# Optimization experiments

Measured on AMD Instinct MI355X. Metric: run time of the kernel, lower is better.

The kernel has to match this reference:

```python
import jax, jax.numpy as jnp
import numpy as np

EPS = 1e-8
TAU = 0.2
IOU_THR = 0.5
NEG = -1e9
N, C, H, D_FG, D_CLS = 8192, 1024, 256, 64, 128


def setup_inputs() -> dict:
    key = jax.random.key(0)
    ks = jax.random.split(key, 11)
    def lin(k, fan_in, fan_out):
        return jax.random.normal(k, (fan_in, fan_out), jnp.float32) / np.sqrt(fan_in)
    return {
        "roi_feats": jax.random.normal(ks[0], (N, C), jnp.float32),
        "labels": jax.random.randint(ks[1], (N,), 0, 21, jnp.int32).astype(jnp.int64),
        "ious": jax.random.uniform(ks[2], (N,), jnp.float32),
        "fg_w1": lin(ks[3], C, H), "fg_b1": jnp.zeros((H,), jnp.float32),
        "fg_w2": lin(ks[4], H, D_FG), "fg_b2": jnp.zeros((D_FG,), jnp.float32),
        "cls_w1": lin(ks[5], C, H), "cls_b1": jnp.zeros((H,), jnp.float32),
        "cls_w2": lin(ks[6], H, D_CLS), "cls_b2": jnp.zeros((D_CLS,), jnp.float32),
    }


def _project_normalize(x, w1, b1, w2, b2):
    h = jax.nn.relu(x @ w1 + b1)
    z = h @ w2 + b2
    norm = jnp.maximum(jnp.linalg.norm(z, axis=1, keepdims=True), EPS)
    return z / norm


def _forward(roi_feats, labels, ious, fg_w1, fg_b1, fg_w2, fg_b2, cls_w1, cls_b1, cls_w2, cls_b2):
    n = roi_feats.shape[0]
    z_fg = _project_normalize(roi_feats, fg_w1, fg_b1, fg_w2, fg_b2)
    z_cls = _project_normalize(roi_feats, cls_w1, cls_b1, cls_w2, cls_b2)

    ignore = labels == -1
    fg = (labels > 0) & ~ignore
    iou_weight = jnp.where(ious > IOU_THR, ious, 0.0)
    eye = jnp.eye(n, dtype=bool)

    # ---- fg/bg contrastive (bg_as_negatives_only=True) ----
    sim_fg = (z_fg @ z_fg.T) / TAU                       # [N,N]
    exp_sim = jnp.exp(sim_fg)
    denom = jnp.sum(exp_sim * (~eye).astype(jnp.float32), axis=1)
    pos = (fg & ~ignore)[None, :] & ~eye                 # positives: fg columns, no self
    n_pos = jnp.sum(pos, axis=1)
    numer = jnp.sum(exp_sim * pos.astype(jnp.float32), axis=1)
    # original computes den = denom + EPS then -log((numer+EPS)/(den+EPS))
    loss_i = -jnp.log((numer + EPS) / (denom + 2.0 * EPS))
    valid = (fg & ~ignore) & (n_pos > 0)
    w = iou_weight * valid.astype(jnp.float32)
    loss_fg_bg = jnp.sum(w * loss_i) / (jnp.sum(w) + EPS)

    # ---- class supervised contrastive ----
    sim_cls = (z_cls @ z_cls.T) / TAU
    sim_masked = jnp.where(eye, NEG, sim_cls)
    log_denom = jax.nn.logsumexp(sim_masked, axis=1)     # [N]
    log_p = jnp.where(eye, NEG, sim_cls - log_denom[:, None])
    # pos_mask keeps diagonal (as in original): same label, col not ignore, col label != 0
    posc = (labels[None, :] == labels[:, None]) & (~ignore)[None, :] & (labels[None, :] != 0)
    n_posc = jnp.sum(posc, axis=1).astype(jnp.float32)
    sum_log_p = jnp.sum(log_p * posc.astype(jnp.float32), axis=1)
    valid_c = (fg & ~ignore) & (n_posc > 0) & jnp.isfinite(log_denom)
    Lzi = jnp.where(valid_c, -sum_log_p / (n_posc + EPS), 0.0)
    wc = iou_weight * valid_c.astype(jnp.float32)
    loss_supcon = jnp.sum(wc * Lzi) / (jnp.sum(wc) + EPS)

    return jnp.stack([loss_fg_bg, loss_supcon])


def reference(roi_feats, labels, ious, fg_w1, fg_b1, fg_w2, fg_b2, cls_w1, cls_b1, cls_w2, cls_b2):
    return _forward(roi_feats, labels, ious, fg_w1, fg_b1, fg_w2, fg_b2, cls_w1, cls_b1, cls_w2, cls_b2)
```

## Files before the change

kernel.cpp:

```cpp
#include <hip/hip_runtime.h>


typedef __attribute__((ext_vector_type(8))) short bs8;
typedef __attribute__((ext_vector_type(4))) float f4;

#define MFMA_BF16(a, b, c) __builtin_amdgcn_mfma_f32_16x16x32_bf16((a), (b), (c), 0, 0, 0)

#if defined(__has_builtin)
#if __has_builtin(__builtin_amdgcn_exp2f)
#define EXP2F(x) __builtin_amdgcn_exp2f(x)
#endif
#endif
#ifndef EXP2F
#define EXP2F(x) exp2f(x)
#endif

#define K_LOG2E 7.2134752044448170f

__device__ __forceinline__ unsigned short f2bf(float f) {
  unsigned int u = __float_as_uint(f);
  u = (u + 0x7fffu + ((u >> 16) & 1u)) >> 16;
  return (unsigned short)u;
}
__device__ __forceinline__ float bf2f(unsigned short s) {
  return __uint_as_float(((unsigned int)s) << 16);
}

constexpr size_t O_W1T  = 0;
constexpr size_t O_W2TF = 1048576;
constexpr size_t O_W2TC = 1081344;
constexpr size_t O_H    = 1146880;
constexpr size_t O_ZF   = 9535488;
constexpr size_t O_ZC   = 10584064;
constexpr size_t O_SCLS = 12681216;
constexpr size_t O_ROWD = 12697600;
constexpr size_t O_ROWN = 12730368;
constexpr size_t O_ROWS = 12763136;
constexpr size_t O_SCAL = 12795904;
constexpr size_t O_HIST = 12795920;
constexpr size_t O_NFG  = 12796048;
constexpr int ZERO_WORDS = (int)((O_NFG + 4 - O_SCLS) / 4);

__global__ void __launch_bounds__(256) zero_kernel(float* __restrict__ p, int n) {
  int i = blockIdx.x * 256 + threadIdx.x;
  if (i < n) p[i] = 0.f;
}

__global__ void __launch_bounds__(256) transp_kernel(
    const float* __restrict__ fgw1, const float* __restrict__ clsw1,
    const float* __restrict__ fgw2, const float* __restrict__ clsw2,
    unsigned short* __restrict__ W1T, unsigned short* __restrict__ W2Tf,
    unsigned short* __restrict__ W2Tc) {
  __shared__ float tile[64][65];
  const int m = blockIdx.y;
  const float* src;
  unsigned short* dst;
  int R, C;
  if (m == 0)      { src = fgw1;  dst = W1T;              R = 1024; C = 256; }
  else if (m == 1) { src = clsw1; dst = W1T + 256 * 1024; R = 1024; C = 256; }
  else if (m == 2) { src = fgw2;  dst = W2Tf;             R = 256;  C = 64;  }
  else             { src = clsw2; dst = W2Tc;             R = 256;  C = 128; }
  const int cT = C >> 6;
  if (blockIdx.x >= (R >> 6) * cT) return;
  const int r0 = (blockIdx.x / cT) << 6, c0 = (blockIdx.x % cT) << 6;
  const int t = threadIdx.x;
  {
    const int rr = t >> 4, cc = (t & 15) << 2;
#pragma unroll
    for (int i = 0; i < 4; i++) {
      float4 v = *(const float4*)(src + (size_t)(r0 + rr + i * 16) * C + c0 + cc);
      tile[rr + i * 16][cc] = v.x; tile[rr + i * 16][cc + 1] = v.y;
      tile[rr + i * 16][cc + 2] = v.z; tile[rr + i * 16][cc + 3] = v.w;
    }
  }
  __syncthreads();
  {
    const int dr = t >> 2, dc = (t & 3) << 4;
    bs8 o0, o1;
#pragma unroll
    for (int j = 0; j < 8; j++) o0[j] = (short)f2bf(tile[dc + j][dr]);
#pragma unroll
    for (int j = 0; j < 8; j++) o1[j] = (short)f2bf(tile[dc + 8 + j][dr]);
    unsigned short* dp = dst + (size_t)(c0 + dr) * R + r0 + dc;
    *(bs8*)dp = o0;
    *(bs8*)(dp + 8) = o1;
  }
}

__global__ void __launch_bounds__(256) meta_kernel(const int* __restrict__ labels,
                                                   int* __restrict__ hist,
                                                   int* __restrict__ nfg) {
  __shared__ int sh[33];
  const int t = threadIdx.x;
  if (t < 33) sh[t] = 0;
  __syncthreads();
  int lab = labels[blockIdx.x * 256 + t];
  if (lab >= 0 && lab < 32) atomicAdd(&sh[lab], 1);
  if (lab > 0) atomicAdd(&sh[32], 1);
  __syncthreads();
  if (t < 32 && sh[t] > 0) atomicAdd(&hist[t], sh[t]);
  if (t == 32 && sh[32] > 0) atomicAdd(nfg, sh[32]);
}

__global__ void __launch_bounds__(256) gemm1_kernel(
    const float* __restrict__ X, const unsigned short* __restrict__ W1T,
    const float* __restrict__ b1f, const float* __restrict__ b1c,
    unsigned short* __restrict__ H) {
  __shared__ __align__(16) unsigned short lA[128 * 40];
  __shared__ __align__(16) unsigned short lB[64 * 40];
  const int t = threadIdx.x;
  const int w = t >> 6, lane = t & 63, ln = lane & 15, quad = lane >> 4;
  const int m0 = blockIdx.x * 128, n0 = blockIdx.y * 64;

  f4 acc[2][4];
#pragma unroll
  for (int rs = 0; rs < 2; rs++)
#pragma unroll
    for (int s = 0; s < 4; s++) acc[rs][s] = (f4){0.f, 0.f, 0.f, 0.f};

  for (int k0 = 0; k0 < 1024; k0 += 32) {
    __syncthreads();
#pragma unroll
    for (int i = 0; i < 2; i++) {
      int ch = t + i * 256;
      int r = ch >> 2, c = (ch & 3) * 8;
      const float* xp = X + (size_t)(m0 + r) * 1024 + k0 + c;
      float4 x0 = *(const float4*)xp;
      float4 x1 = *(const float4*)(xp + 4);
      bs8 av;
      av[0] = (short)f2bf(x0.x); av[1] = (short)f2bf(x0.y);
      av[2] = (short)f2bf(x0.z); av[3] = (short)f2bf(x0.w);
      av[4] = (short)f2bf(x1.x); av[5] = (short)f2bf(x1.y);
      av[6] = (short)f2bf(x1.z); av[7] = (short)f2bf(x1.w);
      *(bs8*)&lA[r * 40 + c] = av;
    }
    {
      int r = t >> 2, c = (t & 3) * 8;
      *(bs8*)&lB[r * 40 + c] = *(const bs8*)(W1T + (size_t)(n0 + r) * 1024 + k0 + c);
    }
    __syncthreads();
    bs8 af0 = *(const bs8*)&lA[(w * 32 + ln) * 40 + quad * 8];
    bs8 af1 = *(const bs8*)&lA[(w * 32 + 16 + ln) * 40 + quad * 8];
#pragma unroll
    for (int s = 0; s < 4; s++) {
      bs8 bf = *(const bs8*)&lB[(s * 16 + ln) * 40 + quad * 8];
      acc[0][s] = MFMA_BF16(af0, bf, acc[0][s]);
      acc[1][s] = MFMA_BF16(af1, bf, acc[1][s]);
    }
  }
#pragma unroll
  for (int s = 0; s < 4; s++) {
    int n = n0 + s * 16 + ln;
    float b = (n < 256) ? b1f[n] : b1c[n - 256];
#pragma unroll
    for (int rs = 0; rs < 2; rs++)
#pragma unroll
      for (int r = 0; r < 4; r++) {
        float v = fmaxf(acc[rs][s][r] + b, 0.f);
        H[(size_t)(m0 + w * 32 + rs * 16 + quad * 4 + r) * 512 + n] = f2bf(v);
      }
  }
}

__global__ void __launch_bounds__(256) gemm2_kernel(
    const unsigned short* __restrict__ H,
    const unsigned short* __restrict__ W2Tf, const unsigned short* __restrict__ W2Tc,
    const float* __restrict__ b2f, const float* __restrict__ b2c,
    unsigned short* __restrict__ Zf, unsigned short* __restrict__ Zc) {
  const int t = threadIdx.x;
  const int w = t >> 6, lane = t & 63, ln = lane & 15, quad = lane >> 4;
  const int rw = blockIdx.x * 32 + (w & 1) * 16;

  if (w < 2) {
    const unsigned short* hrow = H + (size_t)(rw + ln) * 512;
    f4 acc[4];
#pragma unroll
    for (int s = 0; s < 4; s++) acc[s] = (f4){0.f, 0.f, 0.f, 0.f};
#pragma unroll
    for (int ks = 0; ks < 8; ks++) {
      bs8 af = *(const bs8*)(hrow + ks * 32 + quad * 8);
#pragma unroll
      for (int s = 0; s < 4; s++) {
        bs8 bf = *(const bs8*)(W2Tf + (size_t)(s * 16 + ln) * 256 + ks * 32 + quad * 8);
        acc[s] = MFMA_BF16(af, bf, acc[s]);
      }
    }
    float ss[4] = {0.f, 0.f, 0.f, 0.f};
#pragma unroll
    for (int s = 0; s < 4; s++) {
      float b = b2f[s * 16 + ln];
#pragma unroll
      for (int r = 0; r < 4; r++) {
        acc[s][r] += b;
        ss[r] = fmaf(acc[s][r], acc[s][r], ss[r]);
      }
    }
#pragma unroll
    for (int r = 0; r < 4; r++) {
#pragma unroll
      for (int off = 1; off < 16; off <<= 1) ss[r] += __shfl_xor(ss[r], off, 64);
      float sc = 1.f / fmaxf(sqrtf(ss[r]), 1e-8f);
#pragma unroll
      for (int s = 0; s < 4; s++)
        Zf[(size_t)(rw + quad * 4 + r) * 64 + s * 16 + ln] = f2bf(acc[s][r] * sc);
    }
  } else {
    const unsigned short* hrow = H + (size_t)(rw + ln) * 512 + 256;
    f4 acc[8];
#pragma unroll
    for (int s = 0; s < 8; s++) acc[s] = (f4){0.f, 0.f, 0.f, 0.f};
#pragma unroll
    for (int ks = 0; ks < 8; ks++) {
      bs8 af = *(const bs8*)(hrow + ks * 32 + quad * 8);
#pragma unroll
      for (int s = 0; s < 8; s++) {
        bs8 bf = *(const bs8*)(W2Tc + (size_t)(s * 16 + ln) * 256 + ks * 32 + quad * 8);
        acc[s] = MFMA_BF16(af, bf, acc[s]);
      }
    }
    float ss[4] = {0.f, 0.f, 0.f, 0.f};
#pragma unroll
    for (int s = 0; s < 8; s++) {
      float b = b2c[s * 16 + ln];
#pragma unroll
      for (int r = 0; r < 4; r++) {
        acc[s][r] += b;
        ss[r] = fmaf(acc[s][r], acc[s][r], ss[r]);
      }
    }
#pragma unroll
    for (int r = 0; r < 4; r++) {
#pragma unroll
      for (int off = 1; off < 16; off <<= 1) ss[r] += __shfl_xor(ss[r], off, 64);
      float sc = 1.f / fmaxf(sqrtf(ss[r]), 1e-8f);
#pragma unroll
      for (int s = 0; s < 8; s++)
        Zc[(size_t)(rw + quad * 4 + r) * 128 + s * 16 + ln] = f2bf(acc[s][r] * sc);
    }
  }
}

__global__ void __launch_bounds__(128) scls_kernel(const unsigned short* __restrict__ Zc,
                                                   const int* __restrict__ labels,
                                                   float* __restrict__ Scls) {
  const int c = blockIdx.x + 1;
  const int t = threadIdx.x;
  const int r0 = blockIdx.y * 256;
  float acc = 0.f;
#pragma unroll 4
  for (int r = r0; r < r0 + 256; r++) {
    if (labels[r] == c) acc += bf2f(Zc[(size_t)r * 128 + t]);
  }
  atomicAdd(&Scls[c * 128 + t], acc);
}

__global__ void __launch_bounds__(256) sim_kernel(
    const unsigned short* __restrict__ Zf, const unsigned short* __restrict__ Zc,
    const int* __restrict__ labels,
    float* __restrict__ rowD, float* __restrict__ rowN, float* __restrict__ rowS) {
  const int bi = blockIdx.x, d = blockIdx.y;
  if (d == 32 && bi >= 32) return;
  const int bj = (bi + d) & 63;
  const bool diag = (d == 0);

  __shared__ __align__(16) unsigned short sZf[64 * 72];
  __shared__ __align__(16) unsigned short sZc[64 * 136];
  __shared__ float sFg[64];
  __shared__ float sCol[4][2][4][16][3];
  const int t = threadIdx.x;
  const int w = t >> 6, lane = t & 63, ln = lane & 15, quad = lane >> 4;
  const int rbase = bi * 128 + w * 32;

  bs8 afg[2][2], acl[2][4];
  float fgr[2][4];
#pragma unroll
  for (int rs = 0; rs < 2; rs++) {
    const unsigned short* zf = Zf + (size_t)(rbase + rs * 16 + ln) * 64;
    const unsigned short* zc = Zc + (size_t)(rbase + rs * 16 + ln) * 128;
#pragma unroll
    for (int s = 0; s < 2; s++) afg[rs][s] = *(const bs8*)(zf + s * 32 + quad * 8);
#pragma unroll
    for (int s = 0; s < 4; s++) acl[rs][s] = *(const bs8*)(zc + s * 32 + quad * 8);
#pragma unroll
    for (int r = 0; r < 4; r++)
      fgr[rs][r] = (labels[rbase + rs * 16 + quad * 4 + r] > 0) ? 1.f : 0.f;
  }

  float dacc[2][4] = {}, nacc[2][4] = {}, sacc[2][4] = {};
  float cdacc[2][4] = {}, cnacc[2][4] = {}, csacc[2][4] = {};

#pragma unroll
  for (int ct = 0; ct < 2; ct++) {
    const int c0 = bj * 128 + ct * 64;
    __syncthreads();
#pragma unroll
    for (int i = 0; i < 2; i++) {
      int ch = t + i * 256;
      int j = ch >> 3, c8 = (ch & 7) * 8;
      *(bs8*)&sZf[j * 72 + c8] = *(const bs8*)(Zf + (size_t)(c0 + j) * 64 + c8);
    }
#pragma unroll
    for (int i = 0; i < 4; i++) {
      int ch = t + i * 256;
      int j = ch >> 4, c8 = (ch & 15) * 8;
      *(bs8*)&sZc[j * 136 + c8] = *(const bs8*)(Zc + (size_t)(c0 + j) * 128 + c8);
    }
    if (t < 64) sFg[t] = (labels[c0 + t] > 0) ? 1.f : 0.f;
    __syncthreads();

#pragma unroll
    for (int s = 0; s < 4; s++) {
      const int lcol = s * 16 + ln;
      const float fgc = sFg[lcol];
      bs8 b0 = *(const bs8*)&sZf[lcol * 72 + quad * 8];
      bs8 b1 = *(const bs8*)&sZf[lcol * 72 + 32 + quad * 8];
#pragma unroll
      for (int rs = 0; rs < 2; rs++) {
        f4 c = {0.f, 0.f, 0.f, 0.f};
        c = MFMA_BF16(afg[rs][0], b0, c);
        c = MFMA_BF16(afg[rs][1], b1, c);
#pragma unroll
        for (int r = 0; r < 4; r++) {
          float e = EXP2F(c[r] * K_LOG2E);
          dacc[rs][r] += e;
          nacc[rs][r] = fmaf(fgc, e, nacc[rs][r]);
          cdacc[ct][s] += e;
          cnacc[ct][s] = fmaf(fgr[rs][r], e, cnacc[ct][s]);
        }
      }
      bs8 bc0 = *(const bs8*)&sZc[lcol * 136 + quad * 8];
      bs8 bc1 = *(const bs8*)&sZc[lcol * 136 + 32 + quad * 8];
      bs8 bc2 = *(const bs8*)&sZc[lcol * 136 + 64 + quad * 8];
      bs8 bc3 = *(const bs8*)&sZc[lcol * 136 + 96 + quad * 8];
#pragma unroll
      for (int rs = 0; rs < 2; rs++) {
        f4 c = {0.f, 0.f, 0.f, 0.f};
        c = MFMA_BF16(acl[rs][0], bc0, c);
        c = MFMA_BF16(acl[rs][1], bc1, c);
        c = MFMA_BF16(acl[rs][2], bc2, c);
        c = MFMA_BF16(acl[rs][3], bc3, c);
#pragma unroll
        for (int r = 0; r < 4; r++) {
          float e = EXP2F(c[r] * K_LOG2E);
          sacc[rs][r] += e;
          csacc[ct][s] += e;
        }
      }
    }
  }

#pragma unroll
  for (int rs = 0; rs < 2; rs++)
#pragma unroll
    for (int r = 0; r < 4; r++) {
      float dv = dacc[rs][r], nv = nacc[rs][r], sv = sacc[rs][r];
#pragma unroll
      for (int off = 1; off < 16; off <<= 1) {
        dv += __shfl_xor(dv, off, 64);
        nv += __shfl_xor(nv, off, 64);
        sv += __shfl_xor(sv, off, 64);
      }
      if (ln == 0) {
        int row = rbase + rs * 16 + quad * 4 + r;
        atomicAdd(&rowD[row], dv);
        atomicAdd(&rowN[row], nv);
        atomicAdd(&rowS[row], sv);
      }
    }

  if (!diag) {
#pragma unroll
    for (int ct = 0; ct < 2; ct++)
#pragma unroll
      for (int s = 0; s < 4; s++) {
        float dv = cdacc[ct][s], nv = cnacc[ct][s], sv = csacc[ct][s];
#pragma unroll
        for (int off = 16; off < 64; off <<= 1) {
          dv += __shfl_xor(dv, off, 64);
          nv += __shfl_xor(nv, off, 64);
          sv += __shfl_xor(sv, off, 64);
        }
        if (quad == 0) {
          sCol[w][ct][s][ln][0] = dv;
          sCol[w][ct][s][ln][1] = nv;
          sCol[w][ct][s][ln][2] = sv;
        }
      }
    __syncthreads();
    if (t < 128) {
      const int ct = t >> 6, s = (t >> 4) & 3, lm = t & 15;
      float dv = 0.f, nv = 0.f, sv = 0.f;
#pragma unroll
      for (int ww = 0; ww < 4; ww++) {
        dv += sCol[ww][ct][s][lm][0];
        nv += sCol[ww][ct][s][lm][1];
        sv += sCol[ww][ct][s][lm][2];
      }
      const int col = bj * 128 + t;
      atomicAdd(&rowD[col], dv);
      atomicAdd(&rowN[col], nv);
      atomicAdd(&rowS[col], sv);
    }
  }
}

__global__ void __launch_bounds__(256) finalize_kernel(
    const unsigned short* __restrict__ Zf, const unsigned short* __restrict__ Zc,
    const int* __restrict__ labels, const float* __restrict__ ious,
    const float* __restrict__ rowD, const float* __restrict__ rowN,
    const float* __restrict__ rowS, const float* __restrict__ Scls,
    const int* __restrict__ hist, const int* __restrict__ nfg,
    float* __restrict__ scal) {
  __shared__ float red[4][4];
  const int t = threadIdx.x, w = t >> 6, lane = t & 63;
  float aw0 = 0.f, al0 = 0.f, aw1 = 0.f, al1 = 0.f;
  const int NFG = *nfg;
  for (int it = 0; it < 16; it++) {
    const int i = it * 512 + blockIdx.x * 4 + w;
    const int lab = labels[i];
    if (lab > 0 && lab < 32) {
      const float iou = ious[i];
      const float iw = (iou > 0.5f) ? iou : 0.f;
      float dot = 0.f, ssq = 0.f;
#pragma unroll
      for (int p = 0; p < 2; p++) {
        const int k = lane + p * 64;
        const float z = bf2f(Zc[(size_t)i * 128 + k]);
        dot = fmaf(z, Scls[lab * 128 + k], dot);
        ssq = fmaf(z, z, ssq);
      }
      float zf = bf2f(Zf[(size_t)i * 64 + lane]);
      float ssqf = zf * zf;
#pragma unroll
      for (int off = 1; off < 64; off <<= 1) {
        dot += __shfl_xor(dot, off, 64);
        ssq += __shfl_xor(ssq, off, 64);
        ssqf += __shfl_xor(ssqf, off, 64);
      }
      if (lane == 0) {
        const float ef = EXP2F(K_LOG2E * ssqf);
        if (NFG - 1 > 0) {
          const float D = rowD[i] - ef;
          const float Nn = rowN[i] - ef;
          const float loss = logf(D + 2e-8f) - logf(Nn + 1e-8f);
          aw0 += iw;
          al0 += iw * loss;
        }
        const int npc = hist[lab];
        if (npc > 0) {
          const float S = rowS[i] - EXP2F(K_LOG2E * ssq);
          const float logden = logf(S);
          const float slp = (dot - ssq) * 5.0f - (float)(npc - 1) * logden - 1e9f;
          aw1 += iw;
          al1 += iw * (-slp / ((float)npc + 1e-8f));
        }
      }
    }
  }
  if (lane == 0) { red[w][0] = aw0; red[w][1] = al0; red[w][2] = aw1; red[w][3] = al1; }
  __syncthreads();
  if (t < 4) atomicAdd(&scal[t], red[0][t] + red[1][t] + red[2][t] + red[3][t]);
}

__global__ void writeout_kernel(const float* __restrict__ scal, float* __restrict__ out) {
  if (threadIdx.x == 0) {
    out[0] = scal[1] / (scal[0] + 1e-8f);
    out[1] = scal[3] / (scal[2] + 1e-8f);
  }
}

extern "C" void kernel_launch(void* const* d_in, const int* in_sizes, int n_in,
                              void* d_out, int out_size, void* d_ws, size_t ws_size,
                              hipStream_t stream) {
  (void)in_sizes; (void)n_in; (void)out_size; (void)ws_size;
  const float* roi    = (const float*)d_in[0];
  const int*   labels = (const int*)d_in[1];
  const float* ious   = (const float*)d_in[2];
  const float* fgw1   = (const float*)d_in[3];
  const float* fgb1   = (const float*)d_in[4];
  const float* fgw2   = (const float*)d_in[5];
  const float* fgb2   = (const float*)d_in[6];
  const float* clsw1  = (const float*)d_in[7];
  const float* clsb1  = (const float*)d_in[8];
  const float* clsw2  = (const float*)d_in[9];
  const float* clsb2  = (const float*)d_in[10];

  char* ws = (char*)d_ws;
  unsigned short* W1T  = (unsigned short*)(ws + O_W1T);
  unsigned short* W2Tf = (unsigned short*)(ws + O_W2TF);
  unsigned short* W2Tc = (unsigned short*)(ws + O_W2TC);
  unsigned short* Hb   = (unsigned short*)(ws + O_H);
  unsigned short* Zf   = (unsigned short*)(ws + O_ZF);
  unsigned short* Zc   = (unsigned short*)(ws + O_ZC);
  float* Scls = (float*)(ws + O_SCLS);
  float* rowD = (float*)(ws + O_ROWD);
  float* rowN = (float*)(ws + O_ROWN);
  float* rowS = (float*)(ws + O_ROWS);
  float* scal = (float*)(ws + O_SCAL);
  int* hist = (int*)(ws + O_HIST);
  int* nfg  = (int*)(ws + O_NFG);
  float* out = (float*)d_out;

  hipLaunchKernelGGL(zero_kernel, dim3((ZERO_WORDS + 255) / 256), dim3(256), 0, stream,
                     (float*)(ws + O_SCLS), ZERO_WORDS);
  hipLaunchKernelGGL(transp_kernel, dim3(64, 4), dim3(256), 0, stream,
                     fgw1, clsw1, fgw2, clsw2, W1T, W2Tf, W2Tc);
  hipLaunchKernelGGL(meta_kernel, dim3(32), dim3(256), 0, stream, labels, hist, nfg);
  hipLaunchKernelGGL(gemm1_kernel, dim3(64, 8), dim3(256), 0, stream,
                     roi, W1T, fgb1, clsb1, Hb);
  hipLaunchKernelGGL(gemm2_kernel, dim3(256), dim3(256), 0, stream,
                     Hb, W2Tf, W2Tc, fgb2, clsb2, Zf, Zc);
  hipLaunchKernelGGL(scls_kernel, dim3(20, 32), dim3(128), 0, stream, Zc, labels, Scls);
  hipLaunchKernelGGL(sim_kernel, dim3(64, 33), dim3(256), 0, stream,
                     Zf, Zc, labels, rowD, rowN, rowS);
  hipLaunchKernelGGL(finalize_kernel, dim3(128), dim3(256), 0, stream,
                     Zf, Zc, labels, ious, rowD, rowN, rowS, Scls, hist, nfg, scal);
  hipLaunchKernelGGL(writeout_kernel, dim3(1), dim3(64), 0, stream, scal, out);
}
```

Before: 221.9 us.

## Retile gemm1 to 64x128 blocks and merge sim tile pairs per block

gemm1 now uses 64-row by 128-column tiles, so each fp32 X tile is loaded and converted to bf16 only four times instead of eight, at the cost of re-reading more W1T. sim_kernel processes two diagonal offsets per block (grid 64x17 instead of 64x33), so row fragments loaded once are reused across two column tiles and row-partial atomics are halved. This gives fewer, longer blocks, which may reduce occupancy and parallelism. Column reductions are now done per offset inside the loop, which adds extra syncthreads.

```diff
diff --git a/kernel.cpp b/kernel.cpp
--- a/kernel.cpp
+++ b/kernel.cpp
@@ -106,24 +106,20 @@
     const float* __restrict__ X, const unsigned short* __restrict__ W1T,
     const float* __restrict__ b1f, const float* __restrict__ b1c,
     unsigned short* __restrict__ H) {
-  __shared__ __align__(16) unsigned short lA[128 * 40];
-  __shared__ __align__(16) unsigned short lB[64 * 40];
+  __shared__ __align__(16) unsigned short lA[64 * 40];
+  __shared__ __align__(16) unsigned short lB[128 * 40];
   const int t = threadIdx.x;
   const int w = t >> 6, lane = t & 63, ln = lane & 15, quad = lane >> 4;
-  const int m0 = blockIdx.x * 128, n0 = blockIdx.y * 64;
-
-  f4 acc[2][4];
-#pragma unroll
-  for (int rs = 0; rs < 2; rs++)
-#pragma unroll
-    for (int s = 0; s < 4; s++) acc[rs][s] = (f4){0.f, 0.f, 0.f, 0.f};
+  const int m0 = blockIdx.x * 64, n0 = blockIdx.y * 128;
+
+  f4 acc[8];
+#pragma unroll
+  for (int s = 0; s < 8; s++) acc[s] = (f4){0.f, 0.f, 0.f, 0.f};
 
   for (int k0 = 0; k0 < 1024; k0 += 32) {
     __syncthreads();
-#pragma unroll
-    for (int i = 0; i < 2; i++) {
-      int ch = t + i * 256;
-      int r = ch >> 2, c = (ch & 3) * 8;
+    {
+      const int r = t >> 2, c = (t & 3) * 8;
       const float* xp = X + (size_t)(m0 + r) * 1024 + k0 + c;
       float4 x0 = *(const float4*)xp;
       float4 x1 = *(const float4*)(xp + 4);
@@ -134,31 +130,29 @@
       av[6] = (short)f2bf(x1.z); av[7] = (short)f2bf(x1.w);
       *(bs8*)&lA[r * 40 + c] = av;
     }
-    {
-      int r = t >> 2, c = (t & 3) * 8;
+#pragma unroll
+    for (int i = 0; i < 2; i++) {
+      const int ch = t + i * 256;
+      const int r = ch >> 2, c = (ch & 3) * 8;
       *(bs8*)&lB[r * 40 + c] = *(const bs8*)(W1T + (size_t)(n0 + r) * 1024 + k0 + c);
     }
     __syncthreads();
-    bs8 af0 = *(const bs8*)&lA[(w * 32 + ln) * 40 + quad * 8];
-    bs8 af1 = *(const bs8*)&lA[(w * 32 + 16 + ln) * 40 + quad * 8];
-#pragma unroll
-    for (int s = 0; s < 4; s++) {
+    bs8 af = *(const bs8*)&lA[(w * 16 + ln) * 40 + quad * 8];
+#pragma unroll
+    for (int s = 0; s < 8; s++) {
       bs8 bf = *(const bs8*)&lB[(s * 16 + ln) * 40 + quad * 8];
-      acc[0][s] = MFMA_BF16(af0, bf, acc[0][s]);
-      acc[1][s] = MFMA_BF16(af1, bf, acc[1][s]);
-    }
-  }
-#pragma unroll
-  for (int s = 0; s < 4; s++) {
-    int n = n0 + s * 16 + ln;
-    float b = (n < 256) ? b1f[n] : b1c[n - 256];
-#pragma unroll
-    for (int rs = 0; rs < 2; rs++)
-#pragma unroll
-      for (int r = 0; r < 4; r++) {
-        float v = fmaxf(acc[rs][s][r] + b, 0.f);
-        H[(size_t)(m0 + w * 32 + rs * 16 + quad * 4 + r) * 512 + n] = f2bf(v);
-      }
+      acc[s] = MFMA_BF16(af, bf, acc[s]);
+    }
+  }
+#pragma unroll
+  for (int s = 0; s < 8; s++) {
+    const int n = n0 + s * 16 + ln;
+    const float b = (n < 256) ? b1f[n] : b1c[n - 256];
+#pragma unroll
+    for (int r = 0; r < 4; r++) {
+      float v = fmaxf(acc[s][r] + b, 0.f);
+      H[(size_t)(m0 + w * 16 + quad * 4 + r) * 512 + n] = f2bf(v);
+    }
   }
 }
 
@@ -258,10 +252,9 @@
     const unsigned short* __restrict__ Zf, const unsigned short* __restrict__ Zc,
     const int* __restrict__ labels,
     float* __restrict__ rowD, float* __restrict__ rowN, float* __restrict__ rowS) {
-  const int bi = blockIdx.x, d = blockIdx.y;
-  if (d == 32 && bi >= 32) return;
-  const int bj = (bi + d) & 63;
-  const bool diag = (d == 0);
+  const int bi = blockIdx.x, y = blockIdx.y;
+  const int dlo = (y == 0) ? 0 : 2 * y - 1;
+  const int dhi = (y == 0) ? 0 : 2 * y;
 
   __shared__ __align__(16) unsigned short sZf[64 * 72];
   __shared__ __align__(16) unsigned short sZc[64 * 136];
@@ -287,64 +280,105 @@
   }
 
   float dacc[2][4] = {}, nacc[2][4] = {}, sacc[2][4] = {};
-  float cdacc[2][4] = {}, cnacc[2][4] = {}, csacc[2][4] = {};
-
-#pragma unroll
-  for (int ct = 0; ct < 2; ct++) {
-    const int c0 = bj * 128 + ct * 64;
-    __syncthreads();
-#pragma unroll
-    for (int i = 0; i < 2; i++) {
-      int ch = t + i * 256;
-      int j = ch >> 3, c8 = (ch & 7) * 8;
-      *(bs8*)&sZf[j * 72 + c8] = *(const bs8*)(Zf + (size_t)(c0 + j) * 64 + c8);
-    }
-#pragma unroll
-    for (int i = 0; i < 4; i++) {
-      int ch = t + i * 256;
-      int j = ch >> 4, c8 = (ch & 15) * 8;
-      *(bs8*)&sZc[j * 136 + c8] = *(const bs8*)(Zc + (size_t)(c0 + j) * 128 + c8);
-    }
-    if (t < 64) sFg[t] = (labels[c0 + t] > 0) ? 1.f : 0.f;
-    __syncthreads();
-
-#pragma unroll
-    for (int s = 0; s < 4; s++) {
-      const int lcol = s * 16 + ln;
-      const float fgc = sFg[lcol];
-      bs8 b0 = *(const bs8*)&sZf[lcol * 72 + quad * 8];
-      bs8 b1 = *(const bs8*)&sZf[lcol * 72 + 32 + quad * 8];
-#pragma unroll
-      for (int rs = 0; rs < 2; rs++) {
-        f4 c = {0.f, 0.f, 0.f, 0.f};
-        c = MFMA_BF16(afg[rs][0], b0, c);
-        c = MFMA_BF16(afg[rs][1], b1, c);
-#pragma unroll
-        for (int r = 0; r < 4; r++) {
-          float e = EXP2F(c[r] * K_LOG2E);
-          dacc[rs][r] += e;
-          nacc[rs][r] = fmaf(fgc, e, nacc[rs][r]);
-          cdacc[ct][s] += e;
-          cnacc[ct][s] = fmaf(fgr[rs][r], e, cnacc[ct][s]);
+
+  for (int d = dlo; d <= dhi; d++) {
+    if (d == 32 && bi >= 32) break;
+    const int bj = (bi + d) & 63;
+    const bool diag = (d == 0);
+    float cd[2][4] = {}, cn[2][4] = {}, cs[2][4] = {};
+
+#pragma unroll
+    for (int ct = 0; ct < 2; ct++) {
+      const int c0 = bj * 128 + ct * 64;
+      __syncthreads();
+#pragma unroll
+      for (int i = 0; i < 2; i++) {
+        int ch = t + i * 256;
+        int j = ch >> 3, c8 = (ch & 7) * 8;
+        *(bs8*)&sZf[j * 72 + c8] = *(const bs8*)(Zf + (size_t)(c0 + j) * 64 + c8);
+      }
+#pragma unroll
+      for (int i = 0; i < 4; i++) {
+        int ch = t + i * 256;
+        int j = ch >> 4, c8 = (ch & 15) * 8;
+        *(bs8*)&sZc[j * 136 + c8] = *(const bs8*)(Zc + (size_t)(c0 + j) * 128 + c8);
+      }
+      if (t < 64) sFg[t] = (labels[c0 + t] > 0) ? 1.f : 0.f;
+      __syncthreads();
+
+#pragma unroll
+      for (int s = 0; s < 4; s++) {
+        const int lcol = s * 16 + ln;
+        const float fgc = sFg[lcol];
+        bs8 b0 = *(const bs8*)&sZf[lcol * 72 + quad * 8];
+        bs8 b1 = *(const bs8*)&sZf[lcol * 72 + 32 + quad * 8];
+#pragma unroll
+        for (int rs = 0; rs < 2; rs++) {
+          f4 c = {0.f, 0.f, 0.f, 0.f};
+          c = MFMA_BF16(afg[rs][0], b0, c);
+          c = MFMA_BF16(afg[rs][1], b1, c);
+#pragma unroll
+          for (int r = 0; r < 4; r++) {
+            float e = EXP2F(c[r] * K_LOG2E);
+            dacc[rs][r] += e;
+            nacc[rs][r] = fmaf(fgc, e, nacc[rs][r]);
+            cd[ct][s] += e;
+            cn[ct][s] = fmaf(fgr[rs][r], e, cn[ct][s]);
+          }
         }
-      }
-      bs8 bc0 = *(const bs8*)&sZc[lcol * 136 + quad * 8];
-      bs8 bc1 = *(const bs8*)&sZc[lcol * 136 + 32 + quad * 8];
-      bs8 bc2 = *(const bs8*)&sZc[lcol * 136 + 64 + quad * 8];
-      bs8 bc3 = *(const bs8*)&sZc[lcol * 136 + 96 + quad * 8];
-#pragma unroll
-      for (int rs = 0; rs < 2; rs++) {
-        f4 c = {0.f, 0.f, 0.f, 0.f};
-        c = MFMA_BF16(acl[rs][0], bc0, c);
-        c = MFMA_BF16(acl[rs][1], bc1, c);
-        c = MFMA_BF16(acl[rs][2], bc2, c);
-        c = MFMA_BF16(acl[rs][3], bc3, c);
-#pragma unroll
-        for (int r = 0; r < 4; r++) {
-          float e = EXP2F(c[r] * K_LOG2E);
-          sacc[rs][r] += e;
-          csacc[ct][s] += e;
+        bs8 bc0 = *(const bs8*)&sZc[lcol * 136 + quad * 8];
+        bs8 bc1 = *(const bs8*)&sZc[lcol * 136 + 32 + quad * 8];
+        bs8 bc2 = *(const bs8*)&sZc[lcol * 136 + 64 + quad * 8];
+        bs8 bc3 = *(const bs8*)&sZc[lcol * 136 + 96 + quad * 8];
+#pragma unroll
+        for (int rs = 0; rs < 2; rs++) {
+          f4 c = {0.f, 0.f, 0.f, 0.f};
+          c = MFMA_BF16(acl[rs][0], bc0, c);
+          c = MFMA_BF16(acl[rs][1], bc1, c);
+          c = MFMA_BF16(acl[rs][2], bc2, c);
+          c = MFMA_BF16(acl[rs][3], bc3, c);
+#pragma unroll
+          for (int r = 0; r < 4; r++) {
+            float e = EXP2F(c[r] * K_LOG2E);
+            sacc[rs][r] += e;
+            cs[ct][s] += e;
+          }
         }
+      }
+    }
+
+    if (!diag) {
+#pragma unroll
+      for (int ct = 0; ct < 2; ct++)
+#pragma unroll
+        for (int s = 0; s < 4; s++) {
+          float dv = cd[ct][s], nv = cn[ct][s], sv = cs[ct][s];
+#pragma unroll
+          for (int off = 16; off < 64; off <<= 1) {
+            dv += __shfl_xor(dv, off, 64);
+            nv += __shfl_xor(nv, off, 64);
+            sv += __shfl_xor(sv, off, 64);
+          }
+          if (quad == 0) {
+            sCol[w][ct][s][ln][0] = dv;
+            sCol[w][ct][s][ln][1] = nv;
+            sCol[w][ct][s][ln][2] = sv;
+          }
+        }
+      __syncthreads();
+      if (t < 128) {
+        const int ct = t >> 6, s = (t >> 4) & 3, lm = t & 15;
+        float dv = 0.f, nv = 0.f, sv = 0.f;
+#pragma unroll
+        for (int ww = 0; ww < 4; ww++) {
+          dv += sCol[ww][ct][s][lm][0];
+          nv += sCol[ww][ct][s][lm][1];
+          sv += sCol[ww][ct][s][lm][2];
+        }
+        const int col = bj * 128 + t;
+        atomicAdd(&rowD[col], dv);
+        atomicAdd(&rowN[col], nv);
+        atomicAdd(&rowS[col], sv);
       }
     }
   }
@@ -367,41 +401,6 @@
         atomicAdd(&rowS[row], sv);
       }
     }
-
-  if (!diag) {
-#pragma unroll
-    for (int ct = 0; ct < 2; ct++)
-#pragma unroll
-      for (int s = 0; s < 4; s++) {
-        float dv = cdacc[ct][s], nv = cnacc[ct][s], sv = csacc[ct][s];
-#pragma unroll
-        for (int off = 16; off < 64; off <<= 1) {
-          dv += __shfl_xor(dv, off, 64);
-          nv += __shfl_xor(nv, off, 64);
-          sv += __shfl_xor(sv, off, 64);
-        }
-        if (quad == 0) {
-          sCol[w][ct][s][ln][0] = dv;
-          sCol[w][ct][s][ln][1] = nv;
-          sCol[w][ct][s][ln][2] = sv;
-        }
-      }
-    __syncthreads();
-    if (t < 128) {
-      const int ct = t >> 6, s = (t >> 4) & 3, lm = t & 15;
-      float dv = 0.f, nv = 0.f, sv = 0.f;
-#pragma unroll
-      for (int ww = 0; ww < 4; ww++) {
-        dv += sCol[ww][ct][s][lm][0];
-        nv += sCol[ww][ct][s][lm][1];
-        sv += sCol[ww][ct][s][lm][2];
-      }
-      const int col = bj * 128 + t;
-      atomicAdd(&rowD[col], dv);
-      atomicAdd(&rowN[col], nv);
-      atomicAdd(&rowS[col], sv);
-    }
-  }
 }
 
 __global__ void __launch_bounds__(256) finalize_kernel(
@@ -506,12 +505,12 @@
   hipLaunchKernelGGL(transp_kernel, dim3(64, 4), dim3(256), 0, stream,
                      fgw1, clsw1, fgw2, clsw2, W1T, W2Tf, W2Tc);
   hipLaunchKernelGGL(meta_kernel, dim3(32), dim3(256), 0, stream, labels, hist, nfg);
-  hipLaunchKernelGGL(gemm1_kernel, dim3(64, 8), dim3(256), 0, stream,
+  hipLaunchKernelGGL(gemm1_kernel, dim3(128, 4), dim3(256), 0, stream,
                      roi, W1T, fgb1, clsb1, Hb);
   hipLaunchKernelGGL(gemm2_kernel, dim3(256), dim3(256), 0, stream,
                      Hb, W2Tf, W2Tc, fgb2, clsb2, Zf, Zc);
   hipLaunchKernelGGL(scls_kernel, dim3(20, 32), dim3(128), 0, stream, Zc, labels, Scls);
-  hipLaunchKernelGGL(sim_kernel, dim3(64, 33), dim3(256), 0, stream,
+  hipLaunchKernelGGL(sim_kernel, dim3(64, 17), dim3(256), 0, stream,
                      Zf, Zc, labels, rowD, rowN, rowS);
   hipLaunchKernelGGL(finalize_kernel, dim3(128), dim3(256), 0, stream,
                      Zf, Zc, labels, ious, rowD, rowN, rowS, Scls, hist, nfg, scal);
```

Result: slower. 233.9 us (+5.4%).
